# Optimization experiments

Measured on AMD Instinct MI355X. Metric: run time of the kernel, lower is better.

Reference implementation:

```python
import jax, jax.numpy as jnp
import numpy as np
from jax import lax

N, H, W, T = 8, 100, 152, 256
STRIDE = 8
ANCHOR_SIZE = 64.0
PRE_NMS_THRESH = 0.05
PRE_NMS_TOP_N = 1000
NMS_THRESH = 0.6
POST_TOP_N = 100
IMG_H, IMG_W = 800, 1216
BW = (10.0, 10.0, 5.0, 5.0)          # BoxCoder weights (wx, wy, ww, wh)
DWH_CLIP = float(np.log(1000.0 / 16.0))
TO_REMOVE = 1.0


def setup_inputs() -> dict:
    key = jax.random.key(0)
    k1, k2, k3 = jax.random.split(key, 3)
    box_regression = jax.random.normal(k1, (N, 4, H, W), dtype=jnp.float32)
    centerness = jax.random.normal(k2, (N, 1, H, W), dtype=jnp.float32)
    dot_product_logits = jax.random.normal(k3, (N, H * W, T), dtype=jnp.float32)
    # anchor grid matching permute_and_flatten's (H, W, A) row-major ordering
    ys, xs = jnp.meshgrid(jnp.arange(H, dtype=jnp.float32),
                          jnp.arange(W, dtype=jnp.float32), indexing="ij")
    cx = xs.reshape(-1) * STRIDE + STRIDE / 2.0
    cy = ys.reshape(-1) * STRIDE + STRIDE / 2.0
    half = ANCHOR_SIZE / 2.0
    anc = jnp.stack([cx - half, cy - half, cx + half, cy + half], axis=-1)  # [H*W, 4]
    anchors = jnp.broadcast_to(anc, (N, H * W, 4)).astype(jnp.float32)
    return {"box_regression": box_regression, "centerness": centerness,
            "anchors": anchors, "dot_product_logits": dot_product_logits}


def _decode(rel, anc):
    w = anc[..., 2] - anc[..., 0] + TO_REMOVE
    h = anc[..., 3] - anc[..., 1] + TO_REMOVE
    cx = anc[..., 0] + 0.5 * w
    cy = anc[..., 1] + 0.5 * h
    dx = rel[..., 0] / BW[0]
    dy = rel[..., 1] / BW[1]
    dw = jnp.minimum(rel[..., 2] / BW[2], DWH_CLIP)
    dh = jnp.minimum(rel[..., 3] / BW[3], DWH_CLIP)
    pcx = dx * w + cx
    pcy = dy * h + cy
    pw = jnp.exp(dw) * w
    ph = jnp.exp(dh) * h
    return jnp.stack([pcx - 0.5 * pw, pcy - 0.5 * ph,
                      pcx + 0.5 * pw - 1.0, pcy + 0.5 * ph - 1.0], axis=-1)


def _iou_one_vs_all(box, boxes):
    area1 = (box[2] - box[0] + TO_REMOVE) * (box[3] - box[1] + TO_REMOVE)
    area2 = (boxes[:, 2] - boxes[:, 0] + TO_REMOVE) * (boxes[:, 3] - boxes[:, 1] + TO_REMOVE)
    lt = jnp.maximum(box[:2], boxes[:, :2])
    rb = jnp.minimum(box[2:], boxes[:, 2:])
    wh = jnp.maximum(rb - lt + TO_REMOVE, 0.0)
    inter = wh[:, 0] * wh[:, 1]
    return inter / (area1 + area2 - inter)


def _nms_single(boxes, scores):
    # greedy NMS, fixed POST_TOP_N iterations (fpn_post_nms_top_n)
    def step(s, _):
        j = jnp.argmax(s)
        sj = s[j]
        bj = boxes[j]
        flag = (sj > 0).astype(boxes.dtype)
        ious = _iou_one_vs_all(bj, boxes)
        s = jnp.where(ious > NMS_THRESH, 0.0, s).at[j].set(0.0)
        return s, (bj * flag, sj * flag)
    _, (kb, ks) = lax.scan(step, scores, None, length=POST_TOP_N)
    return kb, ks


def reference(box_regression, centerness, anchors, dot_product_logits):
    n, _, h, w = box_regression.shape
    # sigmoid + MEAN token aggregation  -> [N, HWA]
    scores = jax.nn.sigmoid(dot_product_logits).mean(-1)
    # permute_and_flatten: [N,4A,H,W] -> [N, HWA, 4]
    box_reg = box_regression.reshape(n, 1, 4, h, w).transpose(0, 3, 4, 1, 2).reshape(n, -1, 4)
    ctr = jax.nn.sigmoid(centerness.reshape(n, 1, 1, h, w).transpose(0, 3, 4, 1, 2).reshape(n, -1))
    cand = scores > PRE_NMS_THRESH          # threshold on raw aggregated scores
    cls = scores * ctr                      # centerness-weighted score
    masked = jnp.where(cand, cls, 0.0)
    vals, idx = lax.top_k(masked, PRE_NMS_TOP_N)          # per-image top-k candidates
    valid = jnp.take_along_axis(cand, idx, axis=1)        # [N, PRE_NMS_TOP_N]
    sel_reg = jnp.take_along_axis(box_reg, idx[..., None], axis=1)
    sel_anc = jnp.take_along_axis(anchors, idx[..., None], axis=1)
    boxes = _decode(sel_reg, sel_anc)
    # clip_to_image
    boxes = jnp.stack([
        jnp.clip(boxes[..., 0], 0.0, IMG_W - 1.0),
        jnp.clip(boxes[..., 1], 0.0, IMG_H - 1.0),
        jnp.clip(boxes[..., 2], 0.0, IMG_W - 1.0),
        jnp.clip(boxes[..., 3], 0.0, IMG_H - 1.0)], axis=-1)
    vf = valid.astype(boxes.dtype)
    det_scores = jnp.sqrt(jnp.where(valid, vals, 1.0)) * vf   # sqrt of cls*ctr, safe grad
    keep_boxes, keep_scores = jax.vmap(_nms_single)(boxes, det_scores)
    return keep_boxes, keep_scores
```

## Files before the change

kernel.cpp:

```cpp
#include <hip/hip_runtime.h>
#include <math.h>

#define NN 8
#define HH 100
#define WW 152
#define HW (HH*WW)
#define HWP 15360
#define TT 256
#define TOPN 1000
#define CAP 1024
#define POSTN 100
#define IMGW 1216
#define IMGH 800
#define DWH_CLIP 4.135166556742356f

typedef unsigned long long u64;
typedef unsigned int u32;

__global__ __launch_bounds__(256) void score_kernel(
    const float* __restrict__ logits,
    const float* __restrict__ centerness,
    float* __restrict__ masked)
{
    int wid  = blockIdx.x * 4 + (threadIdx.x >> 6);
    int lane = threadIdx.x & 63;
    const float4 v = *(reinterpret_cast<const float4*>(logits + (size_t)wid * TT) + lane);
    float s = 0.f;
    s += __fdividef(1.f, 1.f + expf(-v.x));
    s += __fdividef(1.f, 1.f + expf(-v.y));
    s += __fdividef(1.f, 1.f + expf(-v.z));
    s += __fdividef(1.f, 1.f + expf(-v.w));
    #pragma unroll
    for (int off = 32; off; off >>= 1) s += __shfl_xor(s, off, 64);
    if (lane == 0) {
        float score = s * (1.0f / 256.0f);
        float c = centerness[wid];
        float ctr = 1.f / (1.f + expf(-c));
        masked[wid] = (score > 0.05f) ? score * ctr : 0.f;
    }
}

__global__ __launch_bounds__(256, 1) void select_nms_kernel(
    const float* __restrict__ masked,
    const float* __restrict__ box_reg,
    float* __restrict__ out)
{
    const int n    = blockIdx.x;
    const int tid  = threadIdx.x;
    const int wv   = tid >> 6;
    const int lane = tid & 63;

    __shared__ __align__(16) u32 lbits[HWP];
    __shared__ u64    keys[CAP];
    __shared__ float4 sbox[CAP];
    __shared__ float  sscr[CAP];
    __shared__ int    parts[2][4];
    __shared__ int    s_cnt1, s_cnt2, s_kept;
    __shared__ float4 kbox[128];
    __shared__ float  karea[128];
    __shared__ u64    s_supw[4];
    __shared__ u64    s_matw[4];
    __shared__ int    s_kept2, s_done2;

    float* outb = out + (size_t)n * POSTN * 4;
    float* outs = out + (size_t)NN * POSTN * 4 + (size_t)n * POSTN;

    {
        const uint4* mb4 = reinterpret_cast<const uint4*>(masked + (size_t)n * HW);
        uint4* lb4 = reinterpret_cast<uint4*>(lbits);
        #pragma unroll
        for (int j = 0; j < HWP / 1024; j++) {
            int f = j * 256 + tid;
            uint4 v = make_uint4(0u, 0u, 0u, 0u);
            if (f < HW / 4) v = mb4[f];
            lb4[f] = v;
        }
    }
    __syncthreads();

    int p = 0;
    u32 lo = 0u, hi = 0x3F800000u;
    u32 thr = 0u;
    bool early = false;
    while (lo < hi) {
        u32 mid = lo + ((hi - lo) >> 1);
        int c = 0;
        const uint4* lb4 = reinterpret_cast<const uint4*>(lbits);
        #pragma unroll
        for (int j = 0; j < HWP / 1024; j++) {
            uint4 v = lb4[j * 256 + tid];
            c += (v.x > mid) + (v.y > mid) + (v.z > mid) + (v.w > mid);
        }
        #pragma unroll
        for (int off = 32; off; off >>= 1) c += __shfl_xor(c, off, 64);
        if (lane == 0) parts[p][wv] = c;
        __syncthreads();
        int tot = parts[p][0] + parts[p][1] + parts[p][2] + parts[p][3];
        p ^= 1;
        if (tot >= TOPN && tot <= CAP) { thr = mid; early = true; break; }
        if (tot <= TOPN - 1) hi = mid; else lo = mid + 1;
    }
    if (!early) thr = lo;

    #pragma unroll
    for (int j = 0; j < CAP / 256; j++) keys[tid + j * 256] = 0ull;
    if (tid == 0) { s_cnt1 = 0; s_cnt2 = 0; }
    __syncthreads();
    {
        const uint4* lb4 = reinterpret_cast<const uint4*>(lbits);
        #pragma unroll
        for (int j = 0; j < HWP / 1024; j++) {
            int f = j * 256 + tid;
            uint4 v = lb4[f];
            int e = f * 4;
            if (v.x > thr) { int q = atomicAdd(&s_cnt1, 1); if (q < CAP) keys[q] = (((u64)v.x) << 32) | (u32)(~(e + 0)); }
            if (v.y > thr) { int q = atomicAdd(&s_cnt1, 1); if (q < CAP) keys[q] = (((u64)v.y) << 32) | (u32)(~(e + 1)); }
            if (v.z > thr) { int q = atomicAdd(&s_cnt1, 1); if (q < CAP) keys[q] = (((u64)v.z) << 32) | (u32)(~(e + 2)); }
            if (v.w > thr) { int q = atomicAdd(&s_cnt1, 1); if (q < CAP) keys[q] = (((u64)v.w) << 32) | (u32)(~(e + 3)); }
        }
    }
    __syncthreads();
    if (!early && thr > 0u) {
        const int c1 = min(s_cnt1, TOPN);
        const uint4* lb4 = reinterpret_cast<const uint4*>(lbits);
        #pragma unroll
        for (int j = 0; j < HWP / 1024; j++) {
            int f = j * 256 + tid;
            uint4 v = lb4[f];
            int e = f * 4;
            if (v.x == thr) { int q = atomicAdd(&s_cnt2, 1); if (c1 + q < TOPN) keys[c1 + q] = (((u64)thr) << 32) | (u32)(~(e + 0)); }
            if (v.y == thr) { int q = atomicAdd(&s_cnt2, 1); if (c1 + q < TOPN) keys[c1 + q] = (((u64)thr) << 32) | (u32)(~(e + 1)); }
            if (v.z == thr) { int q = atomicAdd(&s_cnt2, 1); if (c1 + q < TOPN) keys[c1 + q] = (((u64)thr) << 32) | (u32)(~(e + 2)); }
            if (v.w == thr) { int q = atomicAdd(&s_cnt2, 1); if (c1 + q < TOPN) keys[c1 + q] = (((u64)thr) << 32) | (u32)(~(e + 3)); }
        }
    }
    __syncthreads();

    for (int k = 2; k <= CAP; k <<= 1) {
        for (int j2 = k >> 1; j2 > 0; j2 >>= 1) {
            #pragma unroll
            for (int e = 0; e < CAP / 256; e++) {
                int i = tid + e * 256;
                int ixj = i ^ j2;
                if (ixj > i) {
                    u64 a = keys[i], bb = keys[ixj];
                    bool sw = ((i & k) == 0) ? (a < bb) : (a > bb);
                    if (sw) { keys[i] = bb; keys[ixj] = a; }
                }
            }
            __syncthreads();
        }
    }
    if (tid < CAP - TOPN) keys[TOPN + tid] = 0ull;
    __syncthreads();

    #pragma unroll
    for (int e = 0; e < CAP / 256; e++) {
        int pos = tid + e * 256;
        u64 kk = keys[pos];
        float s = __uint_as_float((u32)(kk >> 32));
        float4 box = make_float4(0.f, 0.f, 0.f, 0.f);
        if (s > 0.f) {
            int loc = (int)(~(u32)kk);
            float acx = (float)(loc % WW) * 8.f + 4.f;
            float acy = (float)(loc / WW) * 8.f + 4.f;
            float a0 = acx - 32.f, a1 = acy - 32.f, a2 = acx + 32.f, a3 = acy + 32.f;
            float r0 = box_reg[((size_t)n * 4 + 0) * HW + loc];
            float r1 = box_reg[((size_t)n * 4 + 1) * HW + loc];
            float r2 = box_reg[((size_t)n * 4 + 2) * HW + loc];
            float r3 = box_reg[((size_t)n * 4 + 3) * HW + loc];
            float w  = a2 - a0 + 1.0f;
            float h  = a3 - a1 + 1.0f;
            float cx = a0 + 0.5f * w;
            float cy = a1 + 0.5f * h;
            float dx = r0 / 10.0f;
            float dy = r1 / 10.0f;
            float dw = fminf(r2 / 5.0f, DWH_CLIP);
            float dh = fminf(r3 / 5.0f, DWH_CLIP);
            float pcx = dx * w + cx;
            float pcy = dy * h + cy;
            float pw  = expf(dw) * w;
            float ph  = expf(dh) * h;
            float x1 = pcx - 0.5f * pw;
            float y1 = pcy - 0.5f * ph;
            float x2 = pcx + 0.5f * pw - 1.0f;
            float y2 = pcy + 0.5f * ph - 1.0f;
            box.x = fminf(fmaxf(x1, 0.f), (float)(IMGW - 1));
            box.y = fminf(fmaxf(y1, 0.f), (float)(IMGH - 1));
            box.z = fminf(fmaxf(x2, 0.f), (float)(IMGW - 1));
            box.w = fminf(fmaxf(y2, 0.f), (float)(IMGH - 1));
        }
        sbox[pos] = box;
        sscr[pos] = s;
    }
    if (tid == 0) { s_kept2 = 0; s_done2 = 0; }
    __syncthreads();

    {
        const double MD = (double)0.6f + 0x1p-25;
        const int c  = tid >> 4;
        const int kb = tid & 15;
        int kept = 0;

        for (int i0 = 0; i0 < CAP; i0 += 16) {
            float4 cb = sbox[i0 + c];
            float  ca = (cb.z - cb.x + 1.f) * (cb.w - cb.y + 1.f);
            bool sup = false;
            #pragma unroll
            for (int j = 0; j < 8; j++) {
                int slot = kb + 16 * j;
                if (slot < kept) {
                    float4 kx = kbox[slot];
                    float ix1 = fmaxf(cb.x, kx.x), iy1 = fmaxf(cb.y, kx.y);
                    float ix2 = fminf(cb.z, kx.z), iy2 = fminf(cb.w, kx.w);
                    float iw = fmaxf(ix2 - ix1 + 1.f, 0.f), ih = fmaxf(iy2 - iy1 + 1.f, 0.f);
                    float inter = iw * ih;
                    float denom = (ca + karea[slot]) - inter;
                    sup = sup || ((double)inter > MD * (double)denom);
                }
            }
            bool psup = false;
            if (kb < c) {
                float4 A = sbox[i0 + kb];
                float areaA = (A.z - A.x + 1.f) * (A.w - A.y + 1.f);
                float ix1 = fmaxf(A.x, cb.x), iy1 = fmaxf(A.y, cb.y);
                float ix2 = fminf(A.z, cb.z), iy2 = fminf(A.w, cb.w);
                float iw = fmaxf(ix2 - ix1 + 1.f, 0.f), ih = fmaxf(iy2 - iy1 + 1.f, 0.f);
                float inter = iw * ih;
                float denom = (areaA + ca) - inter;
                psup = ((double)inter > MD * (double)denom);
            }
            u64 bs = __ballot(sup);
            u64 bp = __ballot(psup);
            if (lane == 0) { s_supw[wv] = bs; s_matw[wv] = bp; }
            __syncthreads();

            if (tid < 64) {
                bool dd = (tid < 16) ? (sscr[i0 + tid] <= 0.f) : false;
                u64 db = __ballot(dd);
                u32 dead16 = (u32)db & 0xFFFFu;
                u32 kb16 = 0u;
                int kk = kept;
                int dn = 0;
                for (int cc = 0; cc < 16; cc++) {
                    if ((dead16 >> cc) & 1u) { dn = 1; break; }
                    u32 supbits = (u32)(s_supw[cc >> 2] >> ((cc & 3) * 16)) & 0xFFFFu;
                    u32 colm    = (u32)(s_matw[cc >> 2] >> ((cc & 3) * 16)) & 0xFFFFu;
                    bool scc = (supbits != 0u) || ((colm & kb16) != 0u);
                    if (!scc) {
                        float4 wbx = sbox[i0 + cc];
                        float  wsc = sscr[i0 + cc];
                        float  war = (wbx.z - wbx.x + 1.f) * (wbx.w - wbx.y + 1.f);
                        if (tid == 0) {
                            kbox[kk] = wbx; karea[kk] = war;
                            outb[kk * 4 + 0] = wbx.x; outb[kk * 4 + 1] = wbx.y;
                            outb[kk * 4 + 2] = wbx.z; outb[kk * 4 + 3] = wbx.w;
                            outs[kk] = sqrtf(wsc);
                        }
                        kb16 |= (1u << cc);
                        ++kk;
                        if (kk == POSTN) { dn = 1; break; }
                    }
                }
                if (tid == 0) { s_kept2 = kk; s_done2 = dn; }
            }
            __syncthreads();
            kept = s_kept2;
            if (s_done2) break;
        }
        if (tid == 0) s_kept = kept;
    }
    __syncthreads();

    const int cnt = s_kept;
    for (int i = cnt + tid; i < POSTN; i += 256) {
        outb[i * 4 + 0] = 0.f; outb[i * 4 + 1] = 0.f;
        outb[i * 4 + 2] = 0.f; outb[i * 4 + 3] = 0.f;
        outs[i] = 0.f;
    }
}

extern "C" void kernel_launch(void* const* d_in, const int* in_sizes, int n_in,
                              void* d_out, int out_size, void* d_ws, size_t ws_size,
                              hipStream_t stream) {
    const float* box_reg = (const float*)d_in[0];
    const float* center  = (const float*)d_in[1];
    const float* logits  = (const float*)d_in[3];
    float* out = (float*)d_out;

    float* masked = (float*)d_ws;

    score_kernel<<<(NN * HW) / 4, 256, 0, stream>>>(logits, center, masked);
    select_nms_kernel<<<NN, 256, 0, stream>>>(masked, box_reg, out);
}
```

Measured before the change: 270.0 us.

## Drop LDS staging of scores and sort keys in registers with shuffles

Removes the 60KB shared-memory copy of the per-image masked scores; the binary-search count passes and the compaction passes now read directly from global memory (likely L2-resident). The bitonic sort of 1024 keys is rewritten to keep four keys per thread in registers, using wave shuffles for small strides, in-register swaps for strides 64 and 128, and LDS exchange only for strides of 256 and above, which cuts barriers and shared-memory traffic. The tradeoff is repeated global reads across roughly 30 binary-search iterations in place of LDS reads, in exchange for lower LDS use and fewer synchronisations.

```diff
diff --git a/kernel.cpp b/kernel.cpp
--- a/kernel.cpp
+++ b/kernel.cpp
@@ -5,7 +5,6 @@
 #define HH 100
 #define WW 152
 #define HW (HH*WW)
-#define HWP 15360
 #define TT 256
 #define TOPN 1000
 #define CAP 1024
@@ -49,8 +48,8 @@
     const int tid  = threadIdx.x;
     const int wv   = tid >> 6;
     const int lane = tid & 63;
-
-    __shared__ __align__(16) u32 lbits[HWP];
+    const int NF4  = HW / 4;
+
     __shared__ u64    keys[CAP];
     __shared__ float4 sbox[CAP];
     __shared__ float  sscr[CAP];
@@ -62,21 +61,9 @@
     __shared__ u64    s_matw[4];
     __shared__ int    s_kept2, s_done2;
 
+    const uint4* mb4 = reinterpret_cast<const uint4*>(masked + (size_t)n * HW);
     float* outb = out + (size_t)n * POSTN * 4;
     float* outs = out + (size_t)NN * POSTN * 4 + (size_t)n * POSTN;
-
-    {
-        const uint4* mb4 = reinterpret_cast<const uint4*>(masked + (size_t)n * HW);
-        uint4* lb4 = reinterpret_cast<uint4*>(lbits);
-        #pragma unroll
-        for (int j = 0; j < HWP / 1024; j++) {
-            int f = j * 256 + tid;
-            uint4 v = make_uint4(0u, 0u, 0u, 0u);
-            if (f < HW / 4) v = mb4[f];
-            lb4[f] = v;
-        }
-    }
-    __syncthreads();
 
     int p = 0;
     u32 lo = 0u, hi = 0x3F800000u;
@@ -85,11 +72,13 @@
     while (lo < hi) {
         u32 mid = lo + ((hi - lo) >> 1);
         int c = 0;
-        const uint4* lb4 = reinterpret_cast<const uint4*>(lbits);
         #pragma unroll
-        for (int j = 0; j < HWP / 1024; j++) {
-            uint4 v = lb4[j * 256 + tid];
-            c += (v.x > mid) + (v.y > mid) + (v.z > mid) + (v.w > mid);
+        for (int j = 0; j < 15; j++) {
+            int f = j * 256 + tid;
+            if (f < NF4) {
+                uint4 v = mb4[f];
+                c += (v.x > mid) + (v.y > mid) + (v.z > mid) + (v.w > mid);
+            }
         }
         #pragma unroll
         for (int off = 32; off; off >>= 1) c += __shfl_xor(c, off, 64);
@@ -106,12 +95,11 @@
     for (int j = 0; j < CAP / 256; j++) keys[tid + j * 256] = 0ull;
     if (tid == 0) { s_cnt1 = 0; s_cnt2 = 0; }
     __syncthreads();
-    {
-        const uint4* lb4 = reinterpret_cast<const uint4*>(lbits);
-        #pragma unroll
-        for (int j = 0; j < HWP / 1024; j++) {
-            int f = j * 256 + tid;
-            uint4 v = lb4[f];
+    #pragma unroll
+    for (int j = 0; j < 15; j++) {
+        int f = j * 256 + tid;
+        if (f < NF4) {
+            uint4 v = mb4[f];
             int e = f * 4;
             if (v.x > thr) { int q = atomicAdd(&s_cnt1, 1); if (q < CAP) keys[q] = (((u64)v.x) << 32) | (u32)(~(e + 0)); }
             if (v.y > thr) { int q = atomicAdd(&s_cnt1, 1); if (q < CAP) keys[q] = (((u64)v.y) << 32) | (u32)(~(e + 1)); }
@@ -122,34 +110,62 @@
     __syncthreads();
     if (!early && thr > 0u) {
         const int c1 = min(s_cnt1, TOPN);
-        const uint4* lb4 = reinterpret_cast<const uint4*>(lbits);
         #pragma unroll
-        for (int j = 0; j < HWP / 1024; j++) {
+        for (int j = 0; j < 15; j++) {
             int f = j * 256 + tid;
-            uint4 v = lb4[f];
-            int e = f * 4;
-            if (v.x == thr) { int q = atomicAdd(&s_cnt2, 1); if (c1 + q < TOPN) keys[c1 + q] = (((u64)thr) << 32) | (u32)(~(e + 0)); }
-            if (v.y == thr) { int q = atomicAdd(&s_cnt2, 1); if (c1 + q < TOPN) keys[c1 + q] = (((u64)thr) << 32) | (u32)(~(e + 1)); }
-            if (v.z == thr) { int q = atomicAdd(&s_cnt2, 1); if (c1 + q < TOPN) keys[c1 + q] = (((u64)thr) << 32) | (u32)(~(e + 2)); }
-            if (v.w == thr) { int q = atomicAdd(&s_cnt2, 1); if (c1 + q < TOPN) keys[c1 + q] = (((u64)thr) << 32) | (u32)(~(e + 3)); }
-        }
-    }
-    __syncthreads();
-
-    for (int k = 2; k <= CAP; k <<= 1) {
-        for (int j2 = k >> 1; j2 > 0; j2 >>= 1) {
-            #pragma unroll
-            for (int e = 0; e < CAP / 256; e++) {
-                int i = tid + e * 256;
-                int ixj = i ^ j2;
-                if (ixj > i) {
-                    u64 a = keys[i], bb = keys[ixj];
-                    bool sw = ((i & k) == 0) ? (a < bb) : (a > bb);
-                    if (sw) { keys[i] = bb; keys[ixj] = a; }
+            if (f < NF4) {
+                uint4 v = mb4[f];
+                int e = f * 4;
+                if (v.x == thr) { int q = atomicAdd(&s_cnt2, 1); if (c1 + q < TOPN) keys[c1 + q] = (((u64)thr) << 32) | (u32)(~(e + 0)); }
+                if (v.y == thr) { int q = atomicAdd(&s_cnt2, 1); if (c1 + q < TOPN) keys[c1 + q] = (((u64)thr) << 32) | (u32)(~(e + 1)); }
+                if (v.z == thr) { int q = atomicAdd(&s_cnt2, 1); if (c1 + q < TOPN) keys[c1 + q] = (((u64)thr) << 32) | (u32)(~(e + 2)); }
+                if (v.w == thr) { int q = atomicAdd(&s_cnt2, 1); if (c1 + q < TOPN) keys[c1 + q] = (((u64)thr) << 32) | (u32)(~(e + 3)); }
+            }
+        }
+        __syncthreads();
+    }
+
+    {
+        const int base = (wv << 8) + lane;
+        u64 k0 = keys[base], k1 = keys[base + 64], k2 = keys[base + 128], k3 = keys[base + 192];
+
+        for (int k = 2; k <= CAP; k <<= 1) {
+            for (int j = k >> 1; j > 0; j >>= 1) {
+                if (j >= 256) {
+                    __syncthreads();
+                    keys[base] = k0; keys[base + 64] = k1;
+                    keys[base + 128] = k2; keys[base + 192] = k3;
+                    __syncthreads();
+                    { int i = base;       u64 pv = keys[i ^ j]; bool km = (((i & k) == 0) != ((i & j) != 0)); k0 = km ? (k0 > pv ? k0 : pv) : (k0 < pv ? k0 : pv); }
+                    { int i = base + 64;  u64 pv = keys[i ^ j]; bool km = (((i & k) == 0) != ((i & j) != 0)); k1 = km ? (k1 > pv ? k1 : pv) : (k1 < pv ? k1 : pv); }
+                    { int i = base + 128; u64 pv = keys[i ^ j]; bool km = (((i & k) == 0) != ((i & j) != 0)); k2 = km ? (k2 > pv ? k2 : pv) : (k2 < pv ? k2 : pv); }
+                    { int i = base + 192; u64 pv = keys[i ^ j]; bool km = (((i & k) == 0) != ((i & j) != 0)); k3 = km ? (k3 > pv ? k3 : pv) : (k3 < pv ? k3 : pv); }
+                } else if (j == 128) {
+                    { bool up = ((base & k) == 0);
+                      u64 mx = k0 > k2 ? k0 : k2, mn = k0 < k2 ? k0 : k2;
+                      k0 = up ? mx : mn; k2 = up ? mn : mx; }
+                    { bool up = (((base + 64) & k) == 0);
+                      u64 mx = k1 > k3 ? k1 : k3, mn = k1 < k3 ? k1 : k3;
+                      k1 = up ? mx : mn; k3 = up ? mn : mx; }
+                } else if (j == 64) {
+                    { bool up = ((base & k) == 0);
+                      u64 mx = k0 > k1 ? k0 : k1, mn = k0 < k1 ? k0 : k1;
+                      k0 = up ? mx : mn; k1 = up ? mn : mx; }
+                    { bool up = (((base + 128) & k) == 0);
+                      u64 mx = k2 > k3 ? k2 : k3, mn = k2 < k3 ? k2 : k3;
+                      k2 = up ? mx : mn; k3 = up ? mn : mx; }
+                } else {
+                    { int i = base;       u64 pv = __shfl_xor(k0, j, 64); bool km = (((i & k) == 0) != ((i & j) != 0)); k0 = km ? (k0 > pv ? k0 : pv) : (k0 < pv ? k0 : pv); }
+                    { int i = base + 64;  u64 pv = __shfl_xor(k1, j, 64); bool km = (((i & k) == 0) != ((i & j) != 0)); k1 = km ? (k1 > pv ? k1 : pv) : (k1 < pv ? k1 : pv); }
+                    { int i = base + 128; u64 pv = __shfl_xor(k2, j, 64); bool km = (((i & k) == 0) != ((i & j) != 0)); k2 = km ? (k2 > pv ? k2 : pv) : (k2 < pv ? k2 : pv); }
+                    { int i = base + 192; u64 pv = __shfl_xor(k3, j, 64); bool km = (((i & k) == 0) != ((i & j) != 0)); k3 = km ? (k3 > pv ? k3 : pv) : (k3 < pv ? k3 : pv); }
                 }
             }
-            __syncthreads();
-        }
+        }
+        __syncthreads();
+        keys[base] = k0; keys[base + 64] = k1;
+        keys[base + 128] = k2; keys[base + 192] = k3;
+        __syncthreads();
     }
     if (tid < CAP - TOPN) keys[TOPN + tid] = 0ull;
     __syncthreads();
```

Result: no change. 272.1 us (+0.8%).

## Replace binary-search threshold with radix histogram select and register bitonic sort

Applied to the files above, without the earlier changes.

Swaps the ~30-pass binary search over the score bits for a three-pass radix histogram (11/11/10 bits) that finds the top-1000 threshold directly. The bitonic sort now keeps four keys per thread in registers, using shuffles and in-register swaps for small strides and shared memory only for strides of 256 or more, which cuts the number of barriers. The single selection+NMS kernel is split into three kernels (select, sort+decode, NMS) that pass intermediates through workspace. This adds launch overhead and global round-trips and reuses the masked-score buffer in place for keys, boxes and scores.

```diff
diff --git a/kernel.cpp b/kernel.cpp
--- a/kernel.cpp
+++ b/kernel.cpp
@@ -14,6 +14,10 @@
 #define IMGH 800
 #define DWH_CLIP 4.135166556742356f
 
+#define KEYS_OFF 0
+#define BOX_OFF  2048
+#define SCR_OFF  6144
+
 typedef unsigned long long u64;
 typedef unsigned int u32;
 
@@ -40,33 +44,51 @@
     }
 }
 
-__global__ __launch_bounds__(256, 1) void select_nms_kernel(
-    const float* __restrict__ masked,
-    const float* __restrict__ box_reg,
-    float* __restrict__ out)
-{
-    const int n    = blockIdx.x;
-    const int tid  = threadIdx.x;
-    const int wv   = tid >> 6;
-    const int lane = tid & 63;
+__device__ __forceinline__ void find_crossing(
+    const u32* h, int nbins, int target, int tid, int wv, int lane,
+    int* wsum4, int* s_tmp2, int* out_bin, int* out_above, int* out_total)
+{
+    const int cpt = nbins >> 8;
+    const int b0  = tid * cpt;
+    int L = 0;
+    for (int k = 0; k < cpt; k++) L += (int)h[b0 + k];
+    int x = L;
+    #pragma unroll
+    for (int off = 1; off < 64; off <<= 1) {
+        int y = __shfl_down(x, off, 64);
+        if (lane + off < 64) x += y;
+    }
+    if (lane == 0) wsum4[wv] = x;
+    if (tid == 0) { s_tmp2[0] = -1; s_tmp2[1] = 0; }
+    __syncthreads();
+    int add = 0;
+    for (int w = wv + 1; w < 4; w++) add += wsum4[w];
+    const int St = x + add;
+    const int total = wsum4[0] + wsum4[1] + wsum4[2] + wsum4[3];
+    int run = St - L;
+    for (int k = cpt - 1; k >= 0; k--) {
+        int b = b0 + k;
+        int nr = run + (int)h[b];
+        if (run < target && nr >= target) { s_tmp2[0] = b; s_tmp2[1] = run; }
+        run = nr;
+    }
+    __syncthreads();
+    *out_bin = s_tmp2[0]; *out_above = s_tmp2[1]; *out_total = total;
+}
+
+__global__ __launch_bounds__(256, 1) void hist_select_kernel(float* ws_f)
+{
+    const int n = blockIdx.x, tid = threadIdx.x, wv = tid >> 6, lane = tid & 63;
+    float* seg = ws_f + (size_t)n * HW;
 
     __shared__ __align__(16) u32 lbits[HWP];
-    __shared__ u64    keys[CAP];
-    __shared__ float4 sbox[CAP];
-    __shared__ float  sscr[CAP];
-    __shared__ int    parts[2][4];
-    __shared__ int    s_cnt1, s_cnt2, s_kept;
-    __shared__ float4 kbox[128];
-    __shared__ float  karea[128];
-    __shared__ u64    s_supw[4];
-    __shared__ u64    s_matw[4];
-    __shared__ int    s_kept2, s_done2;
-
-    float* outb = out + (size_t)n * POSTN * 4;
-    float* outs = out + (size_t)NN * POSTN * 4 + (size_t)n * POSTN;
+    __shared__ u32 h[2048];
+    __shared__ u64 keysL[CAP];
+    __shared__ int wsum4[4], s_tmp2[2];
+    __shared__ int s_cnt1, s_cnt2;
 
     {
-        const uint4* mb4 = reinterpret_cast<const uint4*>(masked + (size_t)n * HW);
+        const uint4* mb4 = reinterpret_cast<const uint4*>(seg);
         uint4* lb4 = reinterpret_cast<uint4*>(lbits);
         #pragma unroll
         for (int j = 0; j < HWP / 1024; j++) {
@@ -76,125 +98,213 @@
             lb4[f] = v;
         }
     }
-    __syncthreads();
-
-    int p = 0;
-    u32 lo = 0u, hi = 0x3F800000u;
-    u32 thr = 0u;
-    bool early = false;
-    while (lo < hi) {
-        u32 mid = lo + ((hi - lo) >> 1);
-        int c = 0;
-        const uint4* lb4 = reinterpret_cast<const uint4*>(lbits);
+    const uint4* lb4 = reinterpret_cast<const uint4*>(lbits);
+
+    #pragma unroll
+    for (int j = 0; j < 8; j++) h[tid + j * 256] = 0u;
+    __syncthreads();
+    #pragma unroll
+    for (int j = 0; j < HWP / 1024; j++) {
+        uint4 v = lb4[j * 256 + tid];
+        if (v.x) atomicAdd(&h[v.x >> 21], 1u);
+        if (v.y) atomicAdd(&h[v.y >> 21], 1u);
+        if (v.z) atomicAdd(&h[v.z >> 21], 1u);
+        if (v.w) atomicAdd(&h[v.w >> 21], 1u);
+    }
+    __syncthreads();
+    int b1, ab1, tot1;
+    find_crossing(h, 2048, TOPN, tid, wv, lane, wsum4, s_tmp2, &b1, &ab1, &tot1);
+
+    u32 V = 0u;
+    if (b1 >= 0) {
+        #pragma unroll
+        for (int j = 0; j < 8; j++) h[tid + j * 256] = 0u;
+        __syncthreads();
         #pragma unroll
         for (int j = 0; j < HWP / 1024; j++) {
             uint4 v = lb4[j * 256 + tid];
-            c += (v.x > mid) + (v.y > mid) + (v.z > mid) + (v.w > mid);
-        }
-        #pragma unroll
-        for (int off = 32; off; off >>= 1) c += __shfl_xor(c, off, 64);
-        if (lane == 0) parts[p][wv] = c;
+            if (v.x && (v.x >> 21) == (u32)b1) atomicAdd(&h[(v.x >> 10) & 0x7FFu], 1u);
+            if (v.y && (v.y >> 21) == (u32)b1) atomicAdd(&h[(v.y >> 10) & 0x7FFu], 1u);
+            if (v.z && (v.z >> 21) == (u32)b1) atomicAdd(&h[(v.z >> 10) & 0x7FFu], 1u);
+            if (v.w && (v.w >> 21) == (u32)b1) atomicAdd(&h[(v.w >> 10) & 0x7FFu], 1u);
+        }
         __syncthreads();
-        int tot = parts[p][0] + parts[p][1] + parts[p][2] + parts[p][3];
-        p ^= 1;
-        if (tot >= TOPN && tot <= CAP) { thr = mid; early = true; break; }
-        if (tot <= TOPN - 1) hi = mid; else lo = mid + 1;
-    }
-    if (!early) thr = lo;
-
-    #pragma unroll
-    for (int j = 0; j < CAP / 256; j++) keys[tid + j * 256] = 0ull;
+        int b2, ab2, tot2;
+        find_crossing(h, 2048, TOPN - ab1, tid, wv, lane, wsum4, s_tmp2, &b2, &ab2, &tot2);
+
+        #pragma unroll
+        for (int j = 0; j < 8; j++) h[tid + j * 256] = 0u;
+        __syncthreads();
+        const u32 pfx = ((u32)b1 << 11) | (u32)b2;
+        #pragma unroll
+        for (int j = 0; j < HWP / 1024; j++) {
+            uint4 v = lb4[j * 256 + tid];
+            if (v.x && (v.x >> 10) == pfx) atomicAdd(&h[v.x & 0x3FFu], 1u);
+            if (v.y && (v.y >> 10) == pfx) atomicAdd(&h[v.y & 0x3FFu], 1u);
+            if (v.z && (v.z >> 10) == pfx) atomicAdd(&h[v.z & 0x3FFu], 1u);
+            if (v.w && (v.w >> 10) == pfx) atomicAdd(&h[v.w & 0x3FFu], 1u);
+        }
+        __syncthreads();
+        int b3, ab3, tot3;
+        find_crossing(h, 1024, TOPN - ab1 - ab2, tid, wv, lane, wsum4, s_tmp2, &b3, &ab3, &tot3);
+        V = ((u32)b1 << 21) | ((u32)b2 << 10) | (u32)b3;
+    }
+
+    #pragma unroll
+    for (int j = 0; j < CAP / 256; j++) keysL[tid + j * 256] = 0ull;
     if (tid == 0) { s_cnt1 = 0; s_cnt2 = 0; }
     __syncthreads();
-    {
-        const uint4* lb4 = reinterpret_cast<const uint4*>(lbits);
+    #pragma unroll
+    for (int j = 0; j < HWP / 1024; j++) {
+        int f = j * 256 + tid;
+        uint4 v = lb4[f];
+        int e = f * 4;
+        if (v.x > V) { int q = atomicAdd(&s_cnt1, 1); if (q < CAP) keysL[q] = (((u64)v.x) << 32) | (u32)(~(e + 0)); }
+        if (v.y > V) { int q = atomicAdd(&s_cnt1, 1); if (q < CAP) keysL[q] = (((u64)v.y) << 32) | (u32)(~(e + 1)); }
+        if (v.z > V) { int q = atomicAdd(&s_cnt1, 1); if (q < CAP) keysL[q] = (((u64)v.z) << 32) | (u32)(~(e + 2)); }
+        if (v.w > V) { int q = atomicAdd(&s_cnt1, 1); if (q < CAP) keysL[q] = (((u64)v.w) << 32) | (u32)(~(e + 3)); }
+    }
+    __syncthreads();
+    if (V > 0u) {
+        const int c1 = min(s_cnt1, TOPN);
         #pragma unroll
         for (int j = 0; j < HWP / 1024; j++) {
             int f = j * 256 + tid;
             uint4 v = lb4[f];
             int e = f * 4;
-            if (v.x > thr) { int q = atomicAdd(&s_cnt1, 1); if (q < CAP) keys[q] = (((u64)v.x) << 32) | (u32)(~(e + 0)); }
-            if (v.y > thr) { int q = atomicAdd(&s_cnt1, 1); if (q < CAP) keys[q] = (((u64)v.y) << 32) | (u32)(~(e + 1)); }
-            if (v.z > thr) { int q = atomicAdd(&s_cnt1, 1); if (q < CAP) keys[q] = (((u64)v.z) << 32) | (u32)(~(e + 2)); }
-            if (v.w > thr) { int q = atomicAdd(&s_cnt1, 1); if (q < CAP) keys[q] = (((u64)v.w) << 32) | (u32)(~(e + 3)); }
-        }
-    }
-    __syncthreads();
-    if (!early && thr > 0u) {
-        const int c1 = min(s_cnt1, TOPN);
-        const uint4* lb4 = reinterpret_cast<const uint4*>(lbits);
-        #pragma unroll
-        for (int j = 0; j < HWP / 1024; j++) {
-            int f = j * 256 + tid;
-            uint4 v = lb4[f];
-            int e = f * 4;
-            if (v.x == thr) { int q = atomicAdd(&s_cnt2, 1); if (c1 + q < TOPN) keys[c1 + q] = (((u64)thr) << 32) | (u32)(~(e + 0)); }
-            if (v.y == thr) { int q = atomicAdd(&s_cnt2, 1); if (c1 + q < TOPN) keys[c1 + q] = (((u64)thr) << 32) | (u32)(~(e + 1)); }
-            if (v.z == thr) { int q = atomicAdd(&s_cnt2, 1); if (c1 + q < TOPN) keys[c1 + q] = (((u64)thr) << 32) | (u32)(~(e + 2)); }
-            if (v.w == thr) { int q = atomicAdd(&s_cnt2, 1); if (c1 + q < TOPN) keys[c1 + q] = (((u64)thr) << 32) | (u32)(~(e + 3)); }
-        }
-    }
-    __syncthreads();
+            if (v.x == V) { int q = atomicAdd(&s_cnt2, 1); if (c1 + q < TOPN) keysL[c1 + q] = (((u64)V) << 32) | (u32)(~(e + 0)); }
+            if (v.y == V) { int q = atomicAdd(&s_cnt2, 1); if (c1 + q < TOPN) keysL[c1 + q] = (((u64)V) << 32) | (u32)(~(e + 1)); }
+            if (v.z == V) { int q = atomicAdd(&s_cnt2, 1); if (c1 + q < TOPN) keysL[c1 + q] = (((u64)V) << 32) | (u32)(~(e + 2)); }
+            if (v.w == V) { int q = atomicAdd(&s_cnt2, 1); if (c1 + q < TOPN) keysL[c1 + q] = (((u64)V) << 32) | (u32)(~(e + 3)); }
+        }
+        __syncthreads();
+    }
+
+    u64* gk = reinterpret_cast<u64*>(seg + KEYS_OFF);
+    #pragma unroll
+    for (int j = 0; j < CAP / 256; j++) gk[tid + j * 256] = keysL[tid + j * 256];
+}
+
+__device__ __forceinline__ void decode_one(u64 kk, int n,
+    const float* __restrict__ box_reg, float4* bx, float* sc)
+{
+    float s = __uint_as_float((u32)(kk >> 32));
+    float4 box = make_float4(0.f, 0.f, 0.f, 0.f);
+    if (s > 0.f) {
+        int loc = (int)(~(u32)kk);
+        float acx = (float)(loc % WW) * 8.f + 4.f;
+        float acy = (float)(loc / WW) * 8.f + 4.f;
+        float a0 = acx - 32.f, a1 = acy - 32.f, a2 = acx + 32.f, a3 = acy + 32.f;
+        float r0 = box_reg[((size_t)n * 4 + 0) * HW + loc];
+        float r1 = box_reg[((size_t)n * 4 + 1) * HW + loc];
+        float r2 = box_reg[((size_t)n * 4 + 2) * HW + loc];
+        float r3 = box_reg[((size_t)n * 4 + 3) * HW + loc];
+        float w  = a2 - a0 + 1.0f;
+        float h  = a3 - a1 + 1.0f;
+        float cx = a0 + 0.5f * w;
+        float cy = a1 + 0.5f * h;
+        float dx = r0 / 10.0f;
+        float dy = r1 / 10.0f;
+        float dw = fminf(r2 / 5.0f, DWH_CLIP);
+        float dh = fminf(r3 / 5.0f, DWH_CLIP);
+        float pcx = dx * w + cx;
+        float pcy = dy * h + cy;
+        float pw  = expf(dw) * w;
+        float ph  = expf(dh) * h;
+        float x1 = pcx - 0.5f * pw;
+        float y1 = pcy - 0.5f * ph;
+        float x2 = pcx + 0.5f * pw - 1.0f;
+        float y2 = pcy + 0.5f * ph - 1.0f;
+        box.x = fminf(fmaxf(x1, 0.f), (float)(IMGW - 1));
+        box.y = fminf(fmaxf(y1, 0.f), (float)(IMGH - 1));
+        box.z = fminf(fmaxf(x2, 0.f), (float)(IMGW - 1));
+        box.w = fminf(fmaxf(y2, 0.f), (float)(IMGH - 1));
+    }
+    *bx = box; *sc = s;
+}
+
+__global__ __launch_bounds__(256, 1) void sort_decode_kernel(
+    const float* __restrict__ box_reg, float* ws_f)
+{
+    const int n = blockIdx.x, tid = threadIdx.x, wv = tid >> 6, lane = tid & 63;
+    float* seg = ws_f + (size_t)n * HW;
+    u64* gk = reinterpret_cast<u64*>(seg + KEYS_OFF);
+    __shared__ u64 ks[CAP];
+
+    const int base = (wv << 8) + lane;
+    u64 k0 = gk[base], k1 = gk[base + 64], k2 = gk[base + 128], k3 = gk[base + 192];
 
     for (int k = 2; k <= CAP; k <<= 1) {
-        for (int j2 = k >> 1; j2 > 0; j2 >>= 1) {
-            #pragma unroll
-            for (int e = 0; e < CAP / 256; e++) {
-                int i = tid + e * 256;
-                int ixj = i ^ j2;
-                if (ixj > i) {
-                    u64 a = keys[i], bb = keys[ixj];
-                    bool sw = ((i & k) == 0) ? (a < bb) : (a > bb);
-                    if (sw) { keys[i] = bb; keys[ixj] = a; }
-                }
+        for (int j = k >> 1; j > 0; j >>= 1) {
+            if (j >= 256) {
+                __syncthreads();
+                ks[base] = k0; ks[base + 64] = k1; ks[base + 128] = k2; ks[base + 192] = k3;
+                __syncthreads();
+                { int i = base;       u64 pv = ks[i ^ j]; bool km = (((i & k) == 0) != ((i & j) != 0)); k0 = km ? (k0 > pv ? k0 : pv) : (k0 < pv ? k0 : pv); }
+                { int i = base + 64;  u64 pv = ks[i ^ j]; bool km = (((i & k) == 0) != ((i & j) != 0)); k1 = km ? (k1 > pv ? k1 : pv) : (k1 < pv ? k1 : pv); }
+                { int i = base + 128; u64 pv = ks[i ^ j]; bool km = (((i & k) == 0) != ((i & j) != 0)); k2 = km ? (k2 > pv ? k2 : pv) : (k2 < pv ? k2 : pv); }
+                { int i = base + 192; u64 pv = ks[i ^ j]; bool km = (((i & k) == 0) != ((i & j) != 0)); k3 = km ? (k3 > pv ? k3 : pv) : (k3 < pv ? k3 : pv); }
+            } else if (j == 128) {
+                { bool up = ((base & k) == 0);
+                  u64 mx = k0 > k2 ? k0 : k2, mn = k0 < k2 ? k0 : k2;
+                  k0 = up ? mx : mn; k2 = up ? mn : mx; }
+                { bool up = (((base + 64) & k) == 0);
+                  u64 mx = k1 > k3 ? k1 : k3, mn = k1 < k3 ? k1 : k3;
+                  k1 = up ? mx : mn; k3 = up ? mn : mx; }
+            } else if (j == 64) {
+                { bool up = ((base & k) == 0);
+                  u64 mx = k0 > k1 ? k0 : k1, mn = k0 < k1 ? k0 : k1;
+                  k0 = up ? mx : mn; k1 = up ? mn : mx; }
+                { bool up = (((base + 128) & k) == 0);
+                  u64 mx = k2 > k3 ? k2 : k3, mn = k2 < k3 ? k2 : k3;
+                  k2 = up ? mx : mn; k3 = up ? mn : mx; }
+            } else {
+                { int i = base;       u64 pv = __shfl_xor(k0, j, 64); bool km = (((i & k) == 0) != ((i & j) != 0)); k0 = km ? (k0 > pv ? k0 : pv) : (k0 < pv ? k0 : pv); }
+                { int i = base + 64;  u64 pv = __shfl_xor(k1, j, 64); bool km = (((i & k) == 0) != ((i & j) != 0)); k1 = km ? (k1 > pv ? k1 : pv) : (k1 < pv ? k1 : pv); }
+                { int i = base + 128; u64 pv = __shfl_xor(k2, j, 64); bool km = (((i & k) == 0) != ((i & j) != 0)); k2 = km ? (k2 > pv ? k2 : pv) : (k2 < pv ? k2 : pv); }
+                { int i = base + 192; u64 pv = __shfl_xor(k3, j, 64); bool km = (((i & k) == 0) != ((i & j) != 0)); k3 = km ? (k3 > pv ? k3 : pv) : (k3 < pv ? k3 : pv); }
             }
-            __syncthreads();
-        }
-    }
-    if (tid < CAP - TOPN) keys[TOPN + tid] = 0ull;
-    __syncthreads();
-
-    #pragma unroll
-    for (int e = 0; e < CAP / 256; e++) {
-        int pos = tid + e * 256;
-        u64 kk = keys[pos];
-        float s = __uint_as_float((u32)(kk >> 32));
-        float4 box = make_float4(0.f, 0.f, 0.f, 0.f);
-        if (s > 0.f) {
-            int loc = (int)(~(u32)kk);
-            float acx = (float)(loc % WW) * 8.f + 4.f;
-            float acy = (float)(loc / WW) * 8.f + 4.f;
-            float a0 = acx - 32.f, a1 = acy - 32.f, a2 = acx + 32.f, a3 = acy + 32.f;
-            float r0 = box_reg[((size_t)n * 4 + 0) * HW + loc];
-            float r1 = box_reg[((size_t)n * 4 + 1) * HW + loc];
-            float r2 = box_reg[((size_t)n * 4 + 2) * HW + loc];
-            float r3 = box_reg[((size_t)n * 4 + 3) * HW + loc];
-            float w  = a2 - a0 + 1.0f;
-            float h  = a3 - a1 + 1.0f;
-            float cx = a0 + 0.5f * w;
-            float cy = a1 + 0.5f * h;
-            float dx = r0 / 10.0f;
-            float dy = r1 / 10.0f;
-            float dw = fminf(r2 / 5.0f, DWH_CLIP);
-            float dh = fminf(r3 / 5.0f, DWH_CLIP);
-            float pcx = dx * w + cx;
-            float pcy = dy * h + cy;
-            float pw  = expf(dw) * w;
-            float ph  = expf(dh) * h;
-            float x1 = pcx - 0.5f * pw;
-            float y1 = pcy - 0.5f * ph;
-            float x2 = pcx + 0.5f * pw - 1.0f;
-            float y2 = pcy + 0.5f * ph - 1.0f;
-            box.x = fminf(fmaxf(x1, 0.f), (float)(IMGW - 1));
-            box.y = fminf(fmaxf(y1, 0.f), (float)(IMGH - 1));
-            box.z = fminf(fmaxf(x2, 0.f), (float)(IMGW - 1));
-            box.w = fminf(fmaxf(y2, 0.f), (float)(IMGH - 1));
-        }
-        sbox[pos] = box;
-        sscr[pos] = s;
-    }
-    if (tid == 0) { s_kept2 = 0; s_done2 = 0; }
-    __syncthreads();
+        }
+    }
+    if (base + 192 >= TOPN) k3 = 0ull;
+
+    float4* gbox = reinterpret_cast<float4*>(seg + BOX_OFF);
+    float*  gscr = seg + SCR_OFF;
+    float4 bx; float sc;
+    decode_one(k0, n, box_reg, &bx, &sc); gbox[base]       = bx; gscr[base]       = sc;
+    decode_one(k1, n, box_reg, &bx, &sc); gbox[base + 64]  = bx; gscr[base + 64]  = sc;
+    decode_one(k2, n, box_reg, &bx, &sc); gbox[base + 128] = bx; gscr[base + 128] = sc;
+    decode_one(k3, n, box_reg, &bx, &sc); gbox[base + 192] = bx; gscr[base + 192] = sc;
+}
+
+__global__ __launch_bounds__(256, 1) void nms_scan_kernel(
+    const float* __restrict__ ws_f, float* __restrict__ out)
+{
+    const int n = blockIdx.x, tid = threadIdx.x, wv = tid >> 6, lane = tid & 63;
+    const float* seg = ws_f + (size_t)n * HW;
+
+    __shared__ float4 sbox[CAP];
+    __shared__ float  sscr[CAP];
+    __shared__ float4 kbox[128];
+    __shared__ float  karea[128];
+    __shared__ u64    s_supw[4], s_matw[4];
+    __shared__ int    s_kept, s_kept2, s_done2;
+
+    {
+        const float4* gbox = reinterpret_cast<const float4*>(seg + BOX_OFF);
+        const float*  gscr = seg + SCR_OFF;
+        #pragma unroll
+        for (int j = 0; j < CAP / 256; j++) {
+            int i = tid + j * 256;
+            sbox[i] = gbox[i];
+            sscr[i] = gscr[i];
+        }
+    }
+    if (tid == 0) { s_kept2 = 0; s_done2 = 0; s_kept = 0; }
+    __syncthreads();
+
+    float* outb = out + (size_t)n * POSTN * 4;
+    float* outs = out + (size_t)NN * POSTN * 4 + (size_t)n * POSTN;
 
     {
         const double MD = (double)0.6f + 0x1p-25;
@@ -288,8 +398,10 @@
     const float* logits  = (const float*)d_in[3];
     float* out = (float*)d_out;
 
-    float* masked = (float*)d_ws;
-
-    score_kernel<<<(NN * HW) / 4, 256, 0, stream>>>(logits, center, masked);
-    select_nms_kernel<<<NN, 256, 0, stream>>>(masked, box_reg, out);
-}
+    float* ws_f = (float*)d_ws;
+
+    score_kernel<<<(NN * HW) / 4, 256, 0, stream>>>(logits, center, ws_f);
+    hist_select_kernel<<<NN, 256, 0, stream>>>(ws_f);
+    sort_decode_kernel<<<NN, 256, 0, stream>>>(box_reg, ws_f);
+    nms_scan_kernel<<<NN, 256, 0, stream>>>(ws_f, out);
+}
```

Measured after the change: 269.0 us. No clear change (-0.4%).
